# Performance work log

Measured on AMD Instinct MI355X. Metric: run time of the kernel, lower is better.

Reference implementation:

```python
import jax, jax.numpy as jnp
import numpy as np

N, E, DX, DT, H, C = 100000, 1000000, 126, 2, 8, 16
F_IN = DX + DT          # 128
F_OUT = H * C           # 128
NEG_SLOPE = 0.2


def setup_inputs() -> dict:
    key = jax.random.key(0)
    ks = jax.random.split(key, 12)
    s = 1.0 / np.sqrt(F_IN)
    return {
        "x": jax.random.normal(ks[0], (N, DX), jnp.float32),
        "time_feat": jax.random.normal(ks[1], (N, DT), jnp.float32),
        "edge_index": jax.random.randint(ks[2], (2, E), 0, N, jnp.int64),
        "Wl": jax.random.normal(ks[3], (F_IN, F_OUT), jnp.float32) * s,
        "Wr": jax.random.normal(ks[4], (F_IN, F_OUT), jnp.float32) * s,
        "att": jax.random.normal(ks[5], (H, C), jnp.float32) * 0.25,
        "bias_gat": jax.random.normal(ks[6], (F_OUT,), jnp.float32) * 0.01,
        "Ws": jax.random.normal(ks[7], (F_IN, F_OUT), jnp.float32) * s,
        "bs": jax.random.normal(ks[8], (F_OUT,), jnp.float32) * 0.01,
        "Wo": jax.random.normal(ks[9], (F_OUT, 1), jnp.float32) * (1.0 / np.sqrt(F_OUT)),
        "bo": jax.random.normal(ks[10], (1,), jnp.float32) * 0.01,
    }


def reference(x, time_feat, edge_index, Wl, Wr, att, bias_gat, Ws, bs, Wo, bo):
    raw = jnp.concatenate([x, time_feat], axis=1)            # [N, F_IN]
    n = raw.shape[0]
    # PyG GATv2Conv adds self-loops by default
    loops = jnp.arange(n, dtype=edge_index.dtype)
    src = jnp.concatenate([edge_index[0], loops])             # [E+N]
    dst = jnp.concatenate([edge_index[1], loops])

    xl = (raw @ Wl).reshape(n, H, C)                          # source transform
    xr = (raw @ Wr).reshape(n, H, C)                          # target transform

    m = xl[src] + xr[dst]                                     # [E+N, H, C]
    e = jnp.einsum('ehc,hc->eh', jax.nn.leaky_relu(m, NEG_SLOPE), att)

    # segment softmax over incoming edges of each destination node
    emax = jax.ops.segment_max(e, dst, num_segments=n)        # [N, H]
    ee = jnp.exp(e - emax[dst])
    denom = jax.ops.segment_sum(ee, dst, num_segments=n)
    alpha = ee / (denom[dst] + 1e-16)                         # [E+N, H]

    agg = jax.ops.segment_sum(alpha[:, :, None] * xl[src], dst, num_segments=n)
    graph_x = agg.reshape(n, F_OUT) + bias_gat                # concat heads

    skip_x = raw @ Ws + bs
    combined = jax.nn.elu(graph_x + skip_x)
    return jax.nn.sigmoid(combined @ Wo + bo)                 # [N, 1]
```

## Files before the change

kernel.cpp:

```cpp
#include <hip/hip_runtime.h>
#include <hip/hip_bf16.h>

#define NEG_SLOPE 0.2f
#define LOG2E 1.4426950408889634f
#define MAXDEG 64

typedef __bf16 v8bf __attribute__((ext_vector_type(8)));
typedef float  v4f  __attribute__((ext_vector_type(4)));

static __device__ __forceinline__ unsigned short f2b(float f) {
    unsigned u = __builtin_bit_cast(unsigned, f);
    u += 0x7FFFu + ((u >> 16) & 1u);
    return (unsigned short)(u >> 16);
}
static __device__ __forceinline__ void b2f2(unsigned u, float& lo, float& hi) {
    lo = __builtin_bit_cast(float, u << 16);
    hi = __builtin_bit_cast(float, u & 0xFFFF0000u);
}
static __device__ __forceinline__ void unpack8(uint4 u, float* f) {
    b2f2(u.x, f[0], f[1]); b2f2(u.y, f[2], f[3]);
    b2f2(u.z, f[4], f[5]); b2f2(u.w, f[6], f[7]);
}
static __device__ __forceinline__ int atomIncI(int* p) {
    return __hip_atomic_fetch_add(p, 1, __ATOMIC_RELAXED, __HIP_MEMORY_SCOPE_AGENT);
}

__global__ __launch_bounds__(256) void kA_prep(
    const float* __restrict__ Wl, const float* __restrict__ Wr,
    const float* __restrict__ Ws, unsigned short* __restrict__ Wt,
    int* __restrict__ zero_region, int nzero)
{
    int b = blockIdx.x;
    if (b < 192) {
        int t = b * 256 + threadIdx.x;
        int nn = t >> 7, k = t & 127;
        const float* W = (nn < 128) ? Wl : ((nn < 256) ? Wr : Ws);
        Wt[t] = f2b(W[k * 128 + (nn & 127)]);
    } else {
        int t = (b - 192) * 256 + threadIdx.x;
        if (t < nzero) zero_region[t] = 0;
    }
}

#define KB_HB 512

__global__ __launch_bounds__(256) void kB_build_gemm(
    const int* __restrict__ ei, int E,
    int* __restrict__ counts, int* __restrict__ dense,
    const float* __restrict__ x, const float* __restrict__ tf,
    const unsigned short* __restrict__ Wt,
    const float* __restrict__ bg, const float* __restrict__ bs,
    unsigned short* __restrict__ xl_b, unsigned short* __restrict__ xr_b,
    unsigned short* __restrict__ sk_b, int N)
{
    __shared__ unsigned short lds[12672];
    const int tid = threadIdx.x;

    if (blockIdx.x < KB_HB) {
        const int stride = KB_HB * 256;
        for (int e = blockIdx.x * 256 + tid; e < E; e += stride) {
            int src = ei[e];
            int dst = ei[E + e];
            int r = atomIncI(&counts[dst]);
            if (r < MAXDEG)
                dense[(size_t)dst * MAXDEG + r] = src;
        }
        return;
    }

    const int base = ((int)blockIdx.x - KB_HB) * 32;

    #pragma unroll
    for (int t = 0; t < 8; ++t) {
        int idx = tid + t * 256;
        if (idx < 2016) {
            int row = idx / 63;
            int c = idx - row * 63;
            int gr = base + row; if (gr >= N) gr = N - 1;
            float2 v = *reinterpret_cast<const float2*>(x + (size_t)gr * 126 + 2 * c);
            unsigned u = (unsigned)f2b(v.x) | ((unsigned)f2b(v.y) << 16);
            *reinterpret_cast<unsigned*>(&lds[row * 136 + 2 * c]) = u;
        }
    }
    if (tid < 32) {
        int gr = base + tid; if (gr >= N) gr = N - 1;
        float2 v = *reinterpret_cast<const float2*>(tf + (size_t)gr * 2);
        unsigned u = (unsigned)f2b(v.x) | ((unsigned)f2b(v.y) << 16);
        *reinterpret_cast<unsigned*>(&lds[tid * 136 + 126]) = u;
    }
    __syncthreads();

    const int wv = tid >> 6;
    const int lane = tid & 63;
    const int nidx = lane & 15, quad = lane >> 4;
    const int fbase = wv * 96;

    v4f acc[6][2];
    #pragma unroll
    for (int a = 0; a < 6; ++a)
        #pragma unroll
        for (int b = 0; b < 2; ++b) acc[a][b] = 0.0f;

    #pragma unroll
    for (int ks = 0; ks < 4; ++ks) {
        v8bf bfr[2];
        #pragma unroll
        for (int nf = 0; nf < 2; ++nf)
            bfr[nf] = *reinterpret_cast<const v8bf*>(
                &lds[(nf * 16 + nidx) * 136 + ks * 32 + quad * 8]);
        #pragma unroll
        for (int ft = 0; ft < 6; ++ft) {
            v8bf afr = *reinterpret_cast<const v8bf*>(
                Wt + (size_t)(fbase + ft * 16 + nidx) * 128 + ks * 32 + quad * 8);
            #pragma unroll
            for (int nf = 0; nf < 2; ++nf)
                acc[ft][nf] = __builtin_amdgcn_mfma_f32_16x16x32_bf16(
                    afr, bfr[nf], acc[ft][nf], 0, 0, 0);
        }
    }

    __syncthreads();

    #pragma unroll
    for (int ft = 0; ft < 6; ++ft) {
        const int f = fbase + ft * 16;
        const int arr = f >> 7;
        const int colb = (f & 127) + quad * 4;
        float b0 = 0.0f, b1 = 0.0f, b2 = 0.0f, b3 = 0.0f;
        if (arr == 2) {
            float4 v1 = *reinterpret_cast<const float4*>(bs + (f & 127) + quad * 4);
            float4 v2 = *reinterpret_cast<const float4*>(bg + (f & 127) + quad * 4);
            b0 = v1.x + v2.x; b1 = v1.y + v2.y; b2 = v1.z + v2.z; b3 = v1.w + v2.w;
        }
        #pragma unroll
        for (int nf = 0; nf < 2; ++nf) {
            const int nloc = nf * 16 + nidx;
            v4f v = acc[ft][nf];
            uint2 p;
            p.x = (unsigned)f2b(v[0] + b0) | ((unsigned)f2b(v[1] + b1) << 16);
            p.y = (unsigned)f2b(v[2] + b2) | ((unsigned)f2b(v[3] + b3) << 16);
            *reinterpret_cast<uint2*>(&lds[arr * 4224 + nloc * 132 + colb]) = p;
        }
    }
    __syncthreads();

    #pragma unroll
    for (int it = 0; it < 6; ++it) {
        int i = tid + it * 256;
        int arr = i >> 9;
        int idx = i & 511;
        int nloc = idx >> 4;
        int colh = (idx & 15) * 8;
        int node = base + nloc;
        if (node < N) {
            uint4 v = *reinterpret_cast<const uint4*>(&lds[arr * 4224 + nloc * 132 + colh]);
            unsigned short* dp = (arr == 0) ? xl_b : ((arr == 1) ? xr_b : sk_b);
            *reinterpret_cast<uint4*>(dp + (size_t)node * 128 + colh) = v;
        }
    }
}

__global__ __launch_bounds__(256, 6) void k2_aggfin(
    const int* __restrict__ counts, const int* __restrict__ dense,
    const unsigned short* __restrict__ xl_b,
    const unsigned short* __restrict__ xr_b,
    const unsigned short* __restrict__ sk_b,
    const float* __restrict__ att,
    const float* __restrict__ Wo, const float* __restrict__ bo,
    float* __restrict__ out, int N)
{
    const int node = (int)((blockIdx.x * (size_t)blockDim.x + threadIdx.x) >> 6);
    const int lane = threadIdx.x & 63;
    if (node >= N) return;
    const int j = lane & 15;
    const int g = lane >> 4;
    const int cb = j * 8;

    float4 a0 = *reinterpret_cast<const float4*>(att + cb);
    float4 a1 = *reinterpret_cast<const float4*>(att + cb + 4);
    float av[8] = {a0.x * LOG2E, a0.y * LOG2E, a0.z * LOG2E, a0.w * LOG2E,
                   a1.x * LOG2E, a1.y * LOG2E, a1.z * LOG2E, a1.w * LOG2E};
    float xr[8];
    unpack8(*reinterpret_cast<const uint4*>(xr_b + (size_t)node * 128 + cb), xr);

    float acc[8];
    #pragma unroll
    for (int c = 0; c < 8; ++c) acc[c] = 0.0f;
    float den = 0.0f;

    int cnt = counts[node]; if (cnt > MAXDEG) cnt = MAXDEG;
    const int total = cnt + 1;
    const int* seg = dense + (size_t)node * MAXDEG - 1;

    auto loadsrc = [&](int b0) -> int {
        int ii = b0 + g;
        int ic = (ii > 0 && ii < total) ? ii : 0;
        return (ic == 0) ? node : seg[ic];
    };
    auto gather = [&](int src) -> uint4 {
        return *reinterpret_cast<const uint4*>(xl_b + (size_t)src * 128 + cb);
    };

    int   sB = loadsrc(0);
    uint4 uA = gather(sB);
    sB = loadsrc(4);

    for (int b0 = 0; b0 < total; b0 += 4) {
        uint4 uB = gather(sB);
        int   sC = loadsrc(b0 + 8);

        bool valid = (b0 + g) < total;
        float xl[8];
        unpack8(uA, xl);
        float t = 0.0f;
        #pragma unroll
        for (int c = 0; c < 8; ++c) {
            float m = xl[c] + xr[c];
            float l = fmaxf(m, NEG_SLOPE * m);
            t = fmaf(l, av[c], t);
        }
        t += __shfl_xor(t, 1, 64);
        float e = valid ? exp2f(t) : 0.0f;
        #pragma unroll
        for (int c = 0; c < 8; ++c) acc[c] = fmaf(e, xl[c], acc[c]);
        den += e;

        uA = uB; sB = sC;
    }

    #pragma unroll
    for (int c = 0; c < 8; ++c) {
        acc[c] += __shfl_xor(acc[c], 16, 64);
        acc[c] += __shfl_xor(acc[c], 32, 64);
    }
    den += __shfl_xor(den, 16, 64);
    den += __shfl_xor(den, 32, 64);

    float rd = 1.0f / (den + 1e-16f);
    float sk[8];
    unpack8(*reinterpret_cast<const uint4*>(sk_b + (size_t)node * 128 + cb), sk);
    float4 w0 = *reinterpret_cast<const float4*>(Wo + cb);
    float4 w1 = *reinterpret_cast<const float4*>(Wo + cb + 4);
    float wv[8] = {w0.x, w0.y, w0.z, w0.w, w1.x, w1.y, w1.z, w1.w};
    float s = 0.0f;
    #pragma unroll
    for (int c = 0; c < 8; ++c) {
        float gg = fmaf(acc[c], rd, sk[c]);
        float el = gg > 0.0f ? gg : (exp2f(gg * LOG2E) - 1.0f);
        s = fmaf(el, wv[c], s);
    }
    s += __shfl_xor(s, 1, 64);
    s += __shfl_xor(s, 2, 64);
    s += __shfl_xor(s, 4, 64);
    s += __shfl_xor(s, 8, 64);
    if (lane == 0) {
        float z = s + bo[0];
        out[node] = 1.0f / (1.0f + exp2f(-z * LOG2E));
    }
}

extern "C" void kernel_launch(void* const* d_in, const int* in_sizes, int n_in,
                              void* d_out, int out_size, void* d_ws, size_t ws_size,
                              hipStream_t stream) {
    const float* x   = (const float*)d_in[0];
    const float* tf  = (const float*)d_in[1];
    const int*   ei  = (const int*)  d_in[2];
    const float* Wl  = (const float*)d_in[3];
    const float* Wr  = (const float*)d_in[4];
    const float* att = (const float*)d_in[5];
    const float* bg  = (const float*)d_in[6];
    const float* Ws  = (const float*)d_in[7];
    const float* bs  = (const float*)d_in[8];
    const float* Wo  = (const float*)d_in[9];
    const float* bo  = (const float*)d_in[10];
    float* out = (float*)d_out;

    const int N = in_sizes[0] / 126;
    const int E = in_sizes[2] / 2;

    char* ws = (char*)d_ws;
    unsigned short* Wt   = (unsigned short*)ws; ws += (size_t)384 * 128 * 2;
    unsigned short* xl_b = (unsigned short*)ws; ws += (size_t)N * 128 * 2;
    unsigned short* xr_b = (unsigned short*)ws; ws += (size_t)N * 128 * 2;
    unsigned short* sk_b = (unsigned short*)ws; ws += (size_t)N * 128 * 2;
    int* counts = (int*)ws; ws += (size_t)N * 4;
    int* dense  = (int*)ws; ws += (size_t)N * MAXDEG * 4;

    hipLaunchKernelGGL(kA_prep, dim3(192 + (N + 255) / 256), dim3(256), 0, stream,
                       Wl, Wr, Ws, Wt, counts, N);
    const int GB = (N + 31) / 32;
    hipLaunchKernelGGL(kB_build_gemm, dim3(KB_HB + GB), dim3(256), 0, stream,
                       ei, E, counts, dense, x, tf, Wt, bg, bs,
                       xl_b, xr_b, sk_b, N);
    hipLaunchKernelGGL(k2_aggfin, dim3((N + 3) / 4), dim3(256), 0, stream,
                       counts, dense, xl_b, xr_b, sk_b, att, Wo, bo, out, N);
}
```

Before: 275.7 us.

## Deepen neighbor-gather prefetch, unroll edge-bucketing atomics, zero counts via memset

The aggregation kernel now keeps four gathers of source-feature rows in flight in a ring of slots, instead of the previous single-step prefetch, to hide the latency of random gathers. The edge-bucketing loop handles two edges per iteration so that the independent atomics and index loads can overlap. Zeroing of the counts array moves out of the prep kernel into a hipMemsetAsync, which also makes the prep kernel smaller. The ring is indexed with a runtime slot in a loop that is not unrolled, so the compiler may place the uint4 array in scratch memory, which would add memory traffic to the hot loop.

```diff
diff --git a/kernel.cpp b/kernel.cpp
--- a/kernel.cpp
+++ b/kernel.cpp
@@ -27,19 +27,12 @@
 
 __global__ __launch_bounds__(256) void kA_prep(
     const float* __restrict__ Wl, const float* __restrict__ Wr,
-    const float* __restrict__ Ws, unsigned short* __restrict__ Wt,
-    int* __restrict__ zero_region, int nzero)
+    const float* __restrict__ Ws, unsigned short* __restrict__ Wt)
 {
-    int b = blockIdx.x;
-    if (b < 192) {
-        int t = b * 256 + threadIdx.x;
-        int nn = t >> 7, k = t & 127;
-        const float* W = (nn < 128) ? Wl : ((nn < 256) ? Wr : Ws);
-        Wt[t] = f2b(W[k * 128 + (nn & 127)]);
-    } else {
-        int t = (b - 192) * 256 + threadIdx.x;
-        if (t < nzero) zero_region[t] = 0;
-    }
+    int t = blockIdx.x * 256 + threadIdx.x;
+    int nn = t >> 7, k = t & 127;
+    const float* W = (nn < 128) ? Wl : ((nn < 256) ? Wr : Ws);
+    Wt[t] = f2b(W[k * 128 + (nn & 127)]);
 }
 
 #define KB_HB 512
@@ -58,12 +51,17 @@
 
     if (blockIdx.x < KB_HB) {
         const int stride = KB_HB * 256;
-        for (int e = blockIdx.x * 256 + tid; e < E; e += stride) {
-            int src = ei[e];
-            int dst = ei[E + e];
-            int r = atomIncI(&counts[dst]);
-            if (r < MAXDEG)
-                dense[(size_t)dst * MAXDEG + r] = src;
+        for (int e = blockIdx.x * 256 + tid; e < E; e += 2 * stride) {
+            const int e2 = e + stride;
+            const bool v2 = e2 < E;
+            int src1 = ei[e];
+            int dst1 = ei[E + e];
+            int src2 = 0, dst2 = 0;
+            if (v2) { src2 = ei[e2]; dst2 = ei[E + e2]; }
+            int r1 = atomIncI(&counts[dst1]);
+            int r2 = v2 ? atomIncI(&counts[dst2]) : MAXDEG;
+            if (r1 < MAXDEG) dense[(size_t)dst1 * MAXDEG + r1] = src1;
+            if (r2 < MAXDEG) dense[(size_t)dst2 * MAXDEG + r2] = src2;
         }
         return;
     }
@@ -192,8 +190,8 @@
     const int total = cnt + 1;
     const int* seg = dense + (size_t)node * MAXDEG - 1;
 
-    auto loadsrc = [&](int b0) -> int {
-        int ii = b0 + g;
+    auto loadsrc = [&](int slotbase) -> int {
+        int ii = slotbase + g;
         int ic = (ii > 0 && ii < total) ? ii : 0;
         return (ic == 0) ? node : seg[ic];
     };
@@ -201,17 +199,23 @@
         return *reinterpret_cast<const uint4*>(xl_b + (size_t)src * 128 + cb);
     };
 
-    int   sB = loadsrc(0);
-    uint4 uA = gather(sB);
-    sB = loadsrc(4);
-
-    for (int b0 = 0; b0 < total; b0 += 4) {
-        uint4 uB = gather(sB);
-        int   sC = loadsrc(b0 + 8);
-
-        bool valid = (b0 + g) < total;
+    int   s[4];
+    uint4 u[4];
+    #pragma unroll
+    for (int p = 0; p < 4; ++p) s[p] = loadsrc(p * 4);
+    #pragma unroll
+    for (int p = 0; p < 4; ++p) u[p] = gather(s[p]);
+
+    const int iters = (total + 3) >> 2;
+    for (int it = 0; it < iters; ++it) {
+        const int slot = it & 3;
+        uint4 cur = u[slot];
+        s[slot] = loadsrc((it + 4) * 4);
+        u[slot] = gather(s[slot]);
+
+        bool valid = (it * 4 + g) < total;
         float xl[8];
-        unpack8(uA, xl);
+        unpack8(cur, xl);
         float t = 0.0f;
         #pragma unroll
         for (int c = 0; c < 8; ++c) {
@@ -224,8 +228,6 @@
         #pragma unroll
         for (int c = 0; c < 8; ++c) acc[c] = fmaf(e, xl[c], acc[c]);
         den += e;
-
-        uA = uB; sB = sC;
     }
 
     #pragma unroll
@@ -242,19 +244,19 @@
     float4 w0 = *reinterpret_cast<const float4*>(Wo + cb);
     float4 w1 = *reinterpret_cast<const float4*>(Wo + cb + 4);
     float wv[8] = {w0.x, w0.y, w0.z, w0.w, w1.x, w1.y, w1.z, w1.w};
-    float s = 0.0f;
+    float s2 = 0.0f;
     #pragma unroll
     for (int c = 0; c < 8; ++c) {
         float gg = fmaf(acc[c], rd, sk[c]);
         float el = gg > 0.0f ? gg : (exp2f(gg * LOG2E) - 1.0f);
-        s = fmaf(el, wv[c], s);
-    }
-    s += __shfl_xor(s, 1, 64);
-    s += __shfl_xor(s, 2, 64);
-    s += __shfl_xor(s, 4, 64);
-    s += __shfl_xor(s, 8, 64);
+        s2 = fmaf(el, wv[c], s2);
+    }
+    s2 += __shfl_xor(s2, 1, 64);
+    s2 += __shfl_xor(s2, 2, 64);
+    s2 += __shfl_xor(s2, 4, 64);
+    s2 += __shfl_xor(s2, 8, 64);
     if (lane == 0) {
-        float z = s + bo[0];
+        float z = s2 + bo[0];
         out[node] = 1.0f / (1.0f + exp2f(-z * LOG2E));
     }
 }
@@ -286,8 +288,8 @@
     int* counts = (int*)ws; ws += (size_t)N * 4;
     int* dense  = (int*)ws; ws += (size_t)N * MAXDEG * 4;
 
-    hipLaunchKernelGGL(kA_prep, dim3(192 + (N + 255) / 256), dim3(256), 0, stream,
-                       Wl, Wr, Ws, Wt, counts, N);
+    hipMemsetAsync(counts, 0, (size_t)N * 4, stream);
+    hipLaunchKernelGGL(kA_prep, dim3(192), dim3(256), 0, stream, Wl, Wr, Ws, Wt);
     const int GB = (N + 31) / 32;
     hipLaunchKernelGGL(kB_build_gemm, dim3(KB_HB + GB), dim3(256), 0, stream,
                        ei, E, counts, dense, x, tf, Wt, bg, bs,
```

Result: slower. 303.8 us (+10.2%).
